# Kernel optimization log

Hardware: AMD Instinct MI355X
Metric: run time of the kernel (lower is better)

The kernel has to match this reference:

```python
import jax, jax.numpy as jnp
from jax import lax
import numpy as np

T, B, D = 2048, 16, 1024
INIT_ALPHA_BIAS = 2.0
INIT_D_G = 0.5
INIT_B_G = 0.0


def setup_inputs() -> dict:
    key = jax.random.key(0)
    k_x, k_wa, k_wx = jax.random.split(key, 3)
    scale = 1.0 / np.sqrt(D)  # xavier-ish init for [D,D] weights
    return {
        "x": jax.random.normal(k_x, (T, B, D), dtype=jnp.float32),
        "h0": jnp.zeros((B, D), dtype=jnp.float32),
        "W_alpha": jax.random.normal(k_wa, (D, D), dtype=jnp.float32) * scale,
        "b_alpha": jnp.full((D,), INIT_ALPHA_BIAS, dtype=jnp.float32),
        "W_x": jax.random.normal(k_wx, (D, D), dtype=jnp.float32) * scale,
        "b_v": jnp.zeros((D,), dtype=jnp.float32),
        "d_g": jnp.full((D,), INIT_D_G, dtype=jnp.float32),
        "b_g": jnp.full((D,), INIT_B_G, dtype=jnp.float32),
    }


def reference(x, h0, W_alpha, b_alpha, W_x, b_v, d_g, b_g):
    # Precompute both input projections for all timesteps (one big GEMM each).
    # x @ W.T + b, matching torch Linear-style layout W[dim_out, dim_in].
    alpha_all = jax.nn.sigmoid(jnp.einsum("tbd,ed->tbe", x, W_alpha) + b_alpha)  # [T,B,D]
    v_raw_all = jnp.tanh(jnp.einsum("tbd,ed->tbe", x, W_x) + b_v)                # [T,B,D]

    def step(h_prev, inp):
        alpha, v_raw = inp
        g = jax.nn.sigmoid(d_g * h_prev + b_g)        # self-gating on previous state
        v = v_raw * g
        h_new = alpha * h_prev + (1.0 - alpha) * v
        out = h_new * h_new * jax.nn.sigmoid(h_new)   # h * silu(h)
        return h_new, (out, h_new)

    _, (output, h_seq) = lax.scan(step, h0, (alpha_all, v_raw_all))
    h = jnp.concatenate([h0[None], h_seq], axis=0)    # [T+1,B,D]
    return output, h
```

## Files before the change

kernel.cpp:

```cpp
#include <hip/hip_runtime.h>

typedef unsigned short u16;
typedef unsigned int u32;

#define T_ 2048
#define B_ 16
#define D_ 1024
constexpr int MM = T_ * B_;
constexpr int KK = D_;
constexpr int NN = 2 * D_;
constexpr int BD = B_ * D_;
constexpr int BM = 128, BN = 128, BK = 32;

typedef __bf16 bf16x8 __attribute__((ext_vector_type(8)));
typedef float f32x4 __attribute__((ext_vector_type(4)));

typedef __attribute__((address_space(3))) u32 lds_u32_t;
typedef __attribute__((address_space(1))) u32 gbl_u32_t;

__device__ __forceinline__ void gld16(void* lds, const void* g) {
    __builtin_amdgcn_global_load_lds((const gbl_u32_t*)g, (lds_u32_t*)lds, 16, 0, 0);
}

__device__ __forceinline__ float fast_exp2(float x) {
#if __has_builtin(__builtin_amdgcn_exp2f)
    return __builtin_amdgcn_exp2f(x);
#else
    return exp2f(x);
#endif
}

__device__ inline void split1(float f, u16& h, u16& l) {
    u32 u = __float_as_uint(f);
    h = (u16)(u >> 16);
    float fh = __uint_as_float(u & 0xffff0000u);
    float r = f - fh;
    l = (u16)(__float_as_uint(r) >> 16);
}

__global__ __launch_bounds__(256) void split_kernel(
    const float* __restrict__ src, u16* __restrict__ hi, u16* __restrict__ lo, int n4)
{
    int i = blockIdx.x * 256 + threadIdx.x;
    if (i >= n4) return;
    float4 v = ((const float4*)src)[i];
    u16 h0, h1, h2, h3, l0, l1, l2, l3;
    split1(v.x, h0, l0); split1(v.y, h1, l1);
    split1(v.z, h2, l2); split1(v.w, h3, l3);
    ushort4 hv; hv.x = h0; hv.y = h1; hv.z = h2; hv.w = h3;
    ushort4 lv; lv.x = l0; lv.y = l1; lv.z = l2; lv.w = l3;
    ((ushort4*)hi)[i] = hv;
    ((ushort4*)lo)[i] = lv;
}

__global__ __launch_bounds__(256) void gemm_dual(
    const u16* __restrict__ xhi, const u16* __restrict__ xlo,
    const u16* __restrict__ whi, const u16* __restrict__ wlo,
    const float* __restrict__ ba, const float* __restrict__ bv,
    float* __restrict__ out_ptr, float* __restrict__ h_ptr)
{
    __shared__ u16 Ah[BM][BK];
    __shared__ u16 Al[BM][BK];
    __shared__ u16 Bh[BN][BK];
    __shared__ u16 Bl[BN][BK];

    const int tid  = threadIdx.x;
    const int m0   = blockIdx.y * BM;
    const int n0   = blockIdx.x * BN;
    const int wave = tid >> 6, lane = tid & 63;
    const int wm = (wave & 1) << 6;
    const int wn = (wave >> 1) << 6;
    const int fm = lane & 15, quad = lane >> 4;
    const int wb = wave << 5;
    const int rl = lane >> 2;
    const int cl = (lane & 3) << 3;

    f32x4 acc[4][4] = {};

    for (int k0 = 0; k0 < KK; k0 += BK) {
        size_t ga = (size_t)(m0 + wb + rl) * KK + k0 + cl;
        size_t gb = (size_t)(n0 + wb + rl) * KK + k0 + cl;
        gld16(&Ah[wb][0],      xhi + ga);
        gld16(&Ah[wb + 16][0], xhi + ga + (size_t)16 * KK);
        gld16(&Al[wb][0],      xlo + ga);
        gld16(&Al[wb + 16][0], xlo + ga + (size_t)16 * KK);
        gld16(&Bh[wb][0],      whi + gb);
        gld16(&Bh[wb + 16][0], whi + gb + (size_t)16 * KK);
        gld16(&Bl[wb][0],      wlo + gb);
        gld16(&Bl[wb + 16][0], wlo + gb + (size_t)16 * KK);
        __syncthreads();

        bf16x8 ah[4], al[4], bh[4], bl[4];
        #pragma unroll
        for (int i = 0; i < 4; ++i) {
            ah[i] = *(const bf16x8*)&Ah[wm + i * 16 + fm][quad * 8];
            al[i] = *(const bf16x8*)&Al[wm + i * 16 + fm][quad * 8];
            bh[i] = *(const bf16x8*)&Bh[wn + i * 16 + fm][quad * 8];
            bl[i] = *(const bf16x8*)&Bl[wn + i * 16 + fm][quad * 8];
        }
        #pragma unroll
        for (int mi = 0; mi < 4; ++mi) {
            #pragma unroll
            for (int ni = 0; ni < 4; ++ni) {
                acc[mi][ni] = __builtin_amdgcn_mfma_f32_16x16x32_bf16(ah[mi], bh[ni], acc[mi][ni], 0, 0, 0);
                acc[mi][ni] = __builtin_amdgcn_mfma_f32_16x16x32_bf16(ah[mi], bl[ni], acc[mi][ni], 0, 0, 0);
                acc[mi][ni] = __builtin_amdgcn_mfma_f32_16x16x32_bf16(al[mi], bh[ni], acc[mi][ni], 0, 0, 0);
            }
        }
        __syncthreads();
    }

    const bool is_alpha = (n0 < D_);
    #pragma unroll
    for (int mi = 0; mi < 4; ++mi) {
        #pragma unroll
        for (int ni = 0; ni < 4; ++ni) {
            const int nglob = n0 + wn + ni * 16 + fm;
            #pragma unroll
            for (int r = 0; r < 4; ++r) {
                const int mglob = m0 + wm + mi * 16 + quad * 4 + r;
                float z = acc[mi][ni][r];
                if (is_alpha) {
                    z += ba[nglob];
                    float s = 1.0f / (1.0f + __expf(-z));
                    h_ptr[(size_t)BD + (size_t)mglob * D_ + nglob] = s;
                } else {
                    int nn = nglob - D_;
                    z += bv[nn];
                    out_ptr[(size_t)mglob * D_ + nn] = tanhf(z);
                }
            }
        }
    }
}

#define WAITV(N) asm volatile("s_waitcnt vmcnt(" #N ")" ::: "memory")

__global__ __launch_bounds__(64) void scan_kernel(
    const float* __restrict__ alpha_p,
    const float* __restrict__ vraw_p,
    float* __restrict__ out_p,
    float* __restrict__ hout_p,
    float* __restrict__ h0_dst,
    const float* __restrict__ h0,
    const float* __restrict__ d_g, const float* __restrict__ b_g)
{
    constexpr int PF = 8;
    constexpr int NC = T_ / PF;
    __shared__ float ring[4][2][PF][64];

    const int lane = threadIdx.x;
    const int c0   = blockIdx.x * 64;
    const int i    = c0 + lane;
    const int d    = i & (D_ - 1);
    constexpr float L2E = 1.44269504088896f;
    const float ndg = -d_g[d] * L2E;
    const float nbg = -b_g[d] * L2E;
    float h = h0[i];
    h0_dst[i] = h;

    const float* po = out_p + i;
    const float* dummy = po; (void)dummy;
    float* pov = out_p + i;
    float* phv = hout_p + i;

    const size_t gcol = (size_t)c0 + (size_t)((lane & 15) << 2);
    const int trow = lane >> 4;

#define ISSUE(c_) do {                                                        \
    const int b_ = (c_) & 3;                                                  \
    const size_t t0_ = (size_t)((c_) * PF + trow) * BD + gcol;                \
    gld16(&ring[b_][0][0][0], alpha_p + t0_);                                 \
    gld16(&ring[b_][0][4][0], alpha_p + t0_ + (size_t)4 * BD);                \
    gld16(&ring[b_][1][0][0], vraw_p  + t0_);                                 \
    gld16(&ring[b_][1][4][0], vraw_p  + t0_ + (size_t)4 * BD);                \
} while (0)

#define COMPUTE(c_) do {                                                      \
    const int b_ = (c_) & 3;                                                  \
    _Pragma("unroll")                                                         \
    for (int p = 0; p < PF; ++p) {                                            \
        float a_  = ring[b_][0][p][lane];                                     \
        float vr_ = ring[b_][1][p][lane];                                     \
        float e_  = fast_exp2(__builtin_fmaf(ndg, h, nbg));                   \
        float g_  = __builtin_amdgcn_rcpf(1.0f + e_);                         \
        float v_  = vr_ * g_;                                                 \
        h = __builtin_fmaf(a_, h - v_, v_);                                   \
        float sg_ = __builtin_amdgcn_rcpf(1.0f + fast_exp2(h * -L2E));        \
        const size_t off_ = (size_t)((c_) * PF + p) * BD;                     \
        __builtin_nontemporal_store(h * h * sg_, pov + off_);                 \
        __builtin_nontemporal_store(h, phv + off_);                           \
    }                                                                         \
} while (0)

    ISSUE(0); ISSUE(1); ISSUE(2);

    ISSUE(3); WAITV(8);  COMPUTE(0);
    ISSUE(4); WAITV(24); COMPUTE(1);
    ISSUE(5); WAITV(40); COMPUTE(2);

    for (int c = 3; c < NC - 3; ++c) {
        ISSUE(c + 3);
        WAITV(56);
        COMPUTE(c);
    }

    WAITV(52); COMPUTE(NC - 3);
    WAITV(48); COMPUTE(NC - 2);
    WAITV(44); COMPUTE(NC - 1);

#undef ISSUE
#undef COMPUTE
}

extern "C" void kernel_launch(void* const* d_in, const int* in_sizes, int n_in,
                              void* d_out, int out_size, void* d_ws, size_t ws_size,
                              hipStream_t stream) {
    const float* x  = (const float*)d_in[0];
    const float* h0 = (const float*)d_in[1];
    const float* Wa = (const float*)d_in[2];
    const float* ba = (const float*)d_in[3];
    const float* Wx = (const float*)d_in[4];
    const float* bv = (const float*)d_in[5];
    const float* dg = (const float*)d_in[6];
    const float* bg = (const float*)d_in[7];

    float* out_ptr = (float*)d_out;
    float* h_ptr   = out_ptr + (size_t)T_ * BD;

    u16* xhi = (u16*)d_ws;
    u16* xlo = xhi + (size_t)MM * KK;
    u16* whi = xlo + (size_t)MM * KK;
    u16* wlo = whi + (size_t)NN * KK;

    int n4x = MM * KK / 4;
    split_kernel<<<n4x / 256, 256, 0, stream>>>(x, xhi, xlo, n4x);
    int n4w = D_ * D_ / 4;
    split_kernel<<<n4w / 256, 256, 0, stream>>>(Wa, whi, wlo, n4w);
    split_kernel<<<n4w / 256, 256, 0, stream>>>(Wx, whi + (size_t)D_ * KK, wlo + (size_t)D_ * KK, n4w);

    dim3 grid(NN / BN, MM / BM);
    gemm_dual<<<grid, 256, 0, stream>>>(xhi, xlo, whi, wlo, ba, bv, out_ptr, h_ptr);

    scan_kernel<<<BD / 64, 64, 0, stream>>>(
        h_ptr + BD, out_ptr,
        out_ptr, h_ptr + BD, h_ptr,
        h0, dg, bg);
}
```

Measured before the change: 997.6 us.

## Enlarge GEMM tile to 256x256 with 512 threads and double-buffered LDS

The split-bf16 dual GEMM now uses 256x256 block tiles with 8 waves, each computing a 128x64 sub-tile. LDS is double-buffered so the next K-slice is fetched while MFMAs run on the current one. This raises operand reuse per loaded byte and overlaps global loads with compute. In exchange it uses more registers (32 accumulators per lane), doubles LDS use, and reduces the grid to 1024 blocks, which may limit occupancy.

Result: faster. 945.5 us (-5.2%).

```diff
diff --git a/kernel.cpp b/kernel.cpp
--- a/kernel.cpp
+++ b/kernel.cpp
@@ -10,7 +10,8 @@
 constexpr int KK = D_;
 constexpr int NN = 2 * D_;
 constexpr int BD = B_ * D_;
-constexpr int BM = 128, BN = 128, BK = 32;
+constexpr int BM = 256, BN = 256, BK = 32;
+constexpr int NT = KK / BK;
 
 typedef __bf16 bf16x8 __attribute__((ext_vector_type(8)));
 typedef float f32x4 __attribute__((ext_vector_type(4)));
@@ -53,66 +54,80 @@
     ((ushort4*)lo)[i] = lv;
 }
 
-__global__ __launch_bounds__(256) void gemm_dual(
+__global__ __launch_bounds__(512, 2) void gemm_dual(
     const u16* __restrict__ xhi, const u16* __restrict__ xlo,
     const u16* __restrict__ whi, const u16* __restrict__ wlo,
     const float* __restrict__ ba, const float* __restrict__ bv,
     float* __restrict__ out_ptr, float* __restrict__ h_ptr)
 {
-    __shared__ u16 Ah[BM][BK];
-    __shared__ u16 Al[BM][BK];
-    __shared__ u16 Bh[BN][BK];
-    __shared__ u16 Bl[BN][BK];
+    __shared__ u16 Ah[2][BM][BK];
+    __shared__ u16 Al[2][BM][BK];
+    __shared__ u16 Bh[2][BN][BK];
+    __shared__ u16 Bl[2][BN][BK];
 
     const int tid  = threadIdx.x;
     const int m0   = blockIdx.y * BM;
     const int n0   = blockIdx.x * BN;
     const int wave = tid >> 6, lane = tid & 63;
-    const int wm = (wave & 1) << 6;
-    const int wn = (wave >> 1) << 6;
+    const int wm = (wave >> 2) << 7;
+    const int wn = (wave & 3) << 6;
     const int fm = lane & 15, quad = lane >> 4;
     const int wb = wave << 5;
     const int rl = lane >> 2;
     const int cl = (lane & 3) << 3;
 
-    f32x4 acc[4][4] = {};
-
-    for (int k0 = 0; k0 < KK; k0 += BK) {
-        size_t ga = (size_t)(m0 + wb + rl) * KK + k0 + cl;
-        size_t gb = (size_t)(n0 + wb + rl) * KK + k0 + cl;
-        gld16(&Ah[wb][0],      xhi + ga);
-        gld16(&Ah[wb + 16][0], xhi + ga + (size_t)16 * KK);
-        gld16(&Al[wb][0],      xlo + ga);
-        gld16(&Al[wb + 16][0], xlo + ga + (size_t)16 * KK);
-        gld16(&Bh[wb][0],      whi + gb);
-        gld16(&Bh[wb + 16][0], whi + gb + (size_t)16 * KK);
-        gld16(&Bl[wb][0],      wlo + gb);
-        gld16(&Bl[wb + 16][0], wlo + gb + (size_t)16 * KK);
-        __syncthreads();
-
-        bf16x8 ah[4], al[4], bh[4], bl[4];
+    f32x4 acc[8][4] = {};
+
+    const size_t rowA = (size_t)(m0 + wb + rl) * KK + cl;
+    const size_t rowB = (size_t)(n0 + wb + rl) * KK + cl;
+
+#define STAGE(buf_, k_) do {                                                  \
+    size_t ga = rowA + (size_t)(k_);                                          \
+    size_t gb = rowB + (size_t)(k_);                                          \
+    gld16(&Ah[buf_][wb][0],      xhi + ga);                                   \
+    gld16(&Ah[buf_][wb + 16][0], xhi + ga + (size_t)16 * KK);                 \
+    gld16(&Al[buf_][wb][0],      xlo + ga);                                   \
+    gld16(&Al[buf_][wb + 16][0], xlo + ga + (size_t)16 * KK);                 \
+    gld16(&Bh[buf_][wb][0],      whi + gb);                                   \
+    gld16(&Bh[buf_][wb + 16][0], whi + gb + (size_t)16 * KK);                 \
+    gld16(&Bl[buf_][wb][0],      wlo + gb);                                   \
+    gld16(&Bl[buf_][wb + 16][0], wlo + gb + (size_t)16 * KK);                 \
+} while (0)
+
+    STAGE(0, 0);
+    __syncthreads();
+
+    for (int t = 0; t < NT; ++t) {
+        const int cur = t & 1;
+        if (t + 1 < NT) {
+            const int nxt = cur ^ 1;
+            STAGE(nxt, (t + 1) * BK);
+        }
+
+        bf16x8 bh[4], bl[4];
         #pragma unroll
-        for (int i = 0; i < 4; ++i) {
-            ah[i] = *(const bf16x8*)&Ah[wm + i * 16 + fm][quad * 8];
-            al[i] = *(const bf16x8*)&Al[wm + i * 16 + fm][quad * 8];
-            bh[i] = *(const bf16x8*)&Bh[wn + i * 16 + fm][quad * 8];
-            bl[i] = *(const bf16x8*)&Bl[wn + i * 16 + fm][quad * 8];
+        for (int ni = 0; ni < 4; ++ni) {
+            bh[ni] = *(const bf16x8*)&Bh[cur][wn + ni * 16 + fm][quad * 8];
+            bl[ni] = *(const bf16x8*)&Bl[cur][wn + ni * 16 + fm][quad * 8];
         }
         #pragma unroll
-        for (int mi = 0; mi < 4; ++mi) {
+        for (int mi = 0; mi < 8; ++mi) {
+            bf16x8 ah = *(const bf16x8*)&Ah[cur][wm + mi * 16 + fm][quad * 8];
+            bf16x8 al = *(const bf16x8*)&Al[cur][wm + mi * 16 + fm][quad * 8];
             #pragma unroll
             for (int ni = 0; ni < 4; ++ni) {
-                acc[mi][ni] = __builtin_amdgcn_mfma_f32_16x16x32_bf16(ah[mi], bh[ni], acc[mi][ni], 0, 0, 0);
-                acc[mi][ni] = __builtin_amdgcn_mfma_f32_16x16x32_bf16(ah[mi], bl[ni], acc[mi][ni], 0, 0, 0);
-                acc[mi][ni] = __builtin_amdgcn_mfma_f32_16x16x32_bf16(al[mi], bh[ni], acc[mi][ni], 0, 0, 0);
+                acc[mi][ni] = __builtin_amdgcn_mfma_f32_16x16x32_bf16(ah, bh[ni], acc[mi][ni], 0, 0, 0);
+                acc[mi][ni] = __builtin_amdgcn_mfma_f32_16x16x32_bf16(ah, bl[ni], acc[mi][ni], 0, 0, 0);
+                acc[mi][ni] = __builtin_amdgcn_mfma_f32_16x16x32_bf16(al, bh[ni], acc[mi][ni], 0, 0, 0);
             }
         }
         __syncthreads();
     }
+#undef STAGE
 
     const bool is_alpha = (n0 < D_);
     #pragma unroll
-    for (int mi = 0; mi < 4; ++mi) {
+    for (int mi = 0; mi < 8; ++mi) {
         #pragma unroll
         for (int ni = 0; ni < 4; ++ni) {
             const int nglob = n0 + wn + ni * 16 + fm;
@@ -159,8 +174,6 @@
     float h = h0[i];
     h0_dst[i] = h;
 
-    const float* po = out_p + i;
-    const float* dummy = po; (void)dummy;
     float* pov = out_p + i;
     float* phv = hout_p + i;
 
@@ -240,7 +253,7 @@
     split_kernel<<<n4w / 256, 256, 0, stream>>>(Wx, whi + (size_t)D_ * KK, wlo + (size_t)D_ * KK, n4w);
 
     dim3 grid(NN / BN, MM / BM);
-    gemm_dual<<<grid, 256, 0, stream>>>(xhi, xlo, whi, wlo, ba, bv, out_ptr, h_ptr);
+    gemm_dual<<<grid, 512, 0, stream>>>(xhi, xlo, whi, wlo, ba, bv, out_ptr, h_ptr);
 
     scan_kernel<<<BD / 64, 64, 0, stream>>>(
         h_ptr + BD, out_ptr,
```
